# Performance work log

Measured on AMD Instinct MI355X. Metric: run time of the kernel, lower is better.

## Reference

```python
import jax, jax.numpy as jnp
import numpy as np

N_USERS = 200000
N_ITEMS = 100000
EMB_DIM = 64
N_LAYERS = 3
N_EDGES = 4000000
N_TOTAL = N_USERS + N_ITEMS


def setup_inputs() -> dict:
    key = jax.random.key(0)
    k1, k2, k3, k4 = jax.random.split(key, 4)
    # Xavier-uniform-ish init scale for embeddings
    lim = float(np.sqrt(6.0 / (N_USERS + EMB_DIM)))
    user_w = jax.random.uniform(k1, (N_USERS, EMB_DIM), jnp.float32, -lim, lim)
    lim_i = float(np.sqrt(6.0 / (N_ITEMS + EMB_DIM)))
    item_w = jax.random.uniform(k2, (N_ITEMS, EMB_DIM), jnp.float32, -lim_i, lim_i)
    src = jax.random.randint(k3, (N_EDGES,), 0, N_TOTAL, dtype=jnp.int32)
    dst = jax.random.randint(k4, (N_EDGES,), 0, N_TOTAL, dtype=jnp.int32)
    return {"user_w": user_w, "item_w": item_w, "src": src, "dst": dst}


def reference(user_w, item_w, src, dst):
    # x: [N_TOTAL, D] joint node embedding table
    x = jnp.concatenate([user_w, item_w], axis=0)
    # Row-degree of the COO adjacency (duplicates sum, same as coalesce)
    deg = jax.ops.segment_sum(jnp.ones_like(src, dtype=x.dtype), src,
                              num_segments=N_TOTAL)
    deg_inv_sqrt = jax.lax.rsqrt(deg + 1e-8)
    # Symmetric normalization weight per edge: d_i^-1/2 * d_j^-1/2
    w = (deg_inv_sqrt[src] * deg_inv_sqrt[dst])[:, None]  # [E, 1]

    h = x
    acc = x
    for _ in range(N_LAYERS):
        # SpMM: out[i] = sum_{(i,j) in E} w_ij * h[j]
        h = jax.ops.segment_sum(w * h[dst], src, num_segments=N_TOTAL)
        acc = acc + h
    out = acc / (N_LAYERS + 1)
    return out[:N_USERS], out[N_USERS:]
```

## Files before the change

kernel.cpp:

```cpp
#include <hip/hip_runtime.h>

#define N_USERS  200000
#define N_ITEMS  100000
#define N_TOTAL  300000
#define EMB_DIM  64
#define N_EDGES  4000000
#define N_LAYERS 3

#define SCAN_CHUNK 1024

#define B2_BITS 9
#define B2_ROWS (1 << B2_BITS)
#define NB2 ((N_TOTAL + B2_ROWS - 1) >> B2_BITS)
#define CHUNK_E 8192
#define NBLK ((N_EDGES + CHUNK_E - 1) / CHUNK_E)
#define NFLAT (NB2 * NBLK)
#define NSB_FLAT ((NFLAT + SCAN_CHUNK - 1) / SCAN_CHUNK)

#define DST_BITS 19
#define DST_MASK ((1 << DST_BITS) - 1)

typedef float f32x2 __attribute__((ext_vector_type(2)));

__device__ __forceinline__ unsigned bfpack(float a, float b) {
    unsigned ua = __float_as_uint(a); ua = (ua + 0x7fffu + ((ua >> 16) & 1u)) >> 16;
    unsigned ub = __float_as_uint(b); ub = (ub + 0x7fffu + ((ub >> 16) & 1u)) >> 16;
    return ua | (ub << 16);
}
__device__ __forceinline__ float bflo(unsigned u) { return __uint_as_float(u << 16); }
__device__ __forceinline__ float bfhi(unsigned u) { return __uint_as_float(u & 0xffff0000u); }
__device__ __forceinline__ f32x2 bf2(unsigned u) {
    f32x2 t; t.x = bflo(u); t.y = bfhi(u); return t;
}

__global__ void scanA_g(const int* __restrict__ in, int* __restrict__ out,
                        int* __restrict__ bsums, int n) {
    __shared__ int lds[256];
    int t = threadIdx.x, b = blockIdx.x;
    int base = b * SCAN_CHUNK + t * 4;
    int v[4];
#pragma unroll
    for (int k = 0; k < 4; ++k)
        v[k] = (base + k < n) ? in[base + k] : 0;
    int s = v[0] + v[1] + v[2] + v[3];
    lds[t] = s;
    __syncthreads();
    for (int off = 1; off < 256; off <<= 1) {
        int x = (t >= off) ? lds[t - off] : 0;
        __syncthreads();
        lds[t] += x;
        __syncthreads();
    }
    int inc = lds[t];
    int exc = inc - s;
    if (t == 255) bsums[b] = inc;
    int run = exc;
#pragma unroll
    for (int k = 0; k < 4; ++k) {
        if (base + k < n) out[base + k] = run;
        run += v[k];
    }
}

__global__ void scanB_g(int* __restrict__ bsums, int nb, int* __restrict__ total_out) {
    __shared__ int lds[512];
    int t = threadIdx.x;
    int v = (t < nb) ? bsums[t] : 0;
    lds[t] = v;
    __syncthreads();
    for (int o = 1; o < 512; o <<= 1) {
        int x = (t >= o) ? lds[t - o] : 0;
        __syncthreads();
        lds[t] += x;
        __syncthreads();
    }
    if (t < nb) bsums[t] = lds[t] - v;
    if (total_out && t == nb - 1) *total_out = lds[t];
}

__global__ void scanC_g(int* __restrict__ out, const int* __restrict__ bsums, int n) {
    int i = blockIdx.x * blockDim.x + threadIdx.x;
    if (i < n) out[i] += bsums[i >> 10];
}

__global__ __launch_bounds__(256) void partA_kernel(const int* __restrict__ src,
                                                    int* __restrict__ bcnt) {
    __shared__ int lcnt[NB2];
    int blk = blockIdx.x, t = threadIdx.x;
    for (int i = t; i < NB2; i += 256) lcnt[i] = 0;
    __syncthreads();
    int base = blk * CHUNK_E;
    int end = base + CHUNK_E; if (end > N_EDGES) end = N_EDGES;
    for (int e = base + t; e < end; e += 256)
        atomicAdd(&lcnt[src[e] >> B2_BITS], 1);
    __syncthreads();
    for (int i = t; i < NB2; i += 256)
        bcnt[(size_t)i * NBLK + blk] = lcnt[i];
}

__global__ __launch_bounds__(256) void partC_kernel(const int* __restrict__ src,
                                                    const int* __restrict__ dst,
                                                    const int* __restrict__ boffs,
                                                    int* __restrict__ edgebuf) {
    __shared__ int lcur[NB2];
    int blk = blockIdx.x, t = threadIdx.x;
    for (int i = t; i < NB2; i += 256) lcur[i] = boffs[(size_t)i * NBLK + blk];
    __syncthreads();
    int base = blk * CHUNK_E;
    int end = base + CHUNK_E; if (end > N_EDGES) end = N_EDGES;
    for (int e = base + t; e < end; e += 256) {
        int s = src[e], d = dst[e];
        int pos = atomicAdd(&lcur[s >> B2_BITS], 1);
        edgebuf[pos] = ((s & (B2_ROWS - 1)) << DST_BITS) | d;
    }
}

__global__ __launch_bounds__(256) void part2_kernel(const int* __restrict__ boffs,
                                                    const int* __restrict__ edgebuf,
                                                    int* __restrict__ col,
                                                    int* __restrict__ offs,
                                                    float* __restrict__ dinv) {
    __shared__ int lhist[B2_ROWS];
    __shared__ int lsums[256];
    int b = blockIdx.x;
    int base = b << B2_BITS;
    int nrows = N_TOTAL - base; if (nrows > B2_ROWS) nrows = B2_ROWS;
    int t = threadIdx.x;
    int bstart = boffs[(size_t)b * NBLK];
    int eend = (b + 1 < NB2) ? boffs[(size_t)(b + 1) * NBLK] : N_EDGES;

    for (int i = t; i < B2_ROWS; i += 256) lhist[i] = 0;
    __syncthreads();
    for (int j = bstart + t; j < eend; j += 256)
        atomicAdd(&lhist[edgebuf[j] >> DST_BITS], 1);
    __syncthreads();
    int v0 = lhist[2 * t], v1 = lhist[2 * t + 1];
    int s = v0 + v1;
    lsums[t] = s;
    __syncthreads();
    for (int o = 1; o < 256; o <<= 1) {
        int x = (t >= o) ? lsums[t - o] : 0;
        __syncthreads();
        lsums[t] += x;
        __syncthreads();
    }
    int exc = lsums[t] - s;
    int o0 = bstart + exc;
    int o1 = o0 + v0;
    if (2 * t < nrows) {
        offs[base + 2 * t] = o0;
        dinv[base + 2 * t] = rsqrtf((float)v0 + 1e-8f);
    }
    if (2 * t + 1 < nrows) {
        offs[base + 2 * t + 1] = o1;
        dinv[base + 2 * t + 1] = rsqrtf((float)v1 + 1e-8f);
    }
    if (b == NB2 - 1 && t == 0) offs[N_TOTAL] = N_EDGES;
    lhist[2 * t] = o0;
    lhist[2 * t + 1] = o1;
    __syncthreads();
    for (int j = bstart + t; j < eend; j += 256) {
        int e = edgebuf[j];
        int r = e >> DST_BITS;
        int pos = atomicAdd(&lhist[r], 1);
        col[pos] = e & DST_MASK;
    }
}

__global__ void convert_kernel(const float2* __restrict__ uw2,
                               const float2* __restrict__ iw2,
                               const float* __restrict__ dinv,
                               unsigned* __restrict__ g0) {
    int i = blockIdx.x * blockDim.x + threadIdx.x;
    const int n = (N_TOTAL + 1) * 32;
    if (i < n) {
        int row = i >> 5;
        if (row >= N_TOTAL) {
            g0[i] = 0u;
        } else {
            float2 x = (row < N_USERS) ? uw2[i] : iw2[i - N_USERS * 32];
            float di = dinv[row];
            g0[i] = bfpack(di * x.x, di * x.y);
        }
    }
}

template <int MODE>
__global__ __launch_bounds__(256) void gather_kernel(
        const int* __restrict__ offs,
        const int* __restrict__ col,
        const float* __restrict__ dinv,
        const unsigned* __restrict__ gprev,
        unsigned* __restrict__ gnext,
        float4* __restrict__ out4,
        const float4* __restrict__ uw4,
        const float4* __restrict__ iw4) {
    int row  = blockIdx.x * 4 + (threadIdx.x >> 6);
    int lane = threadIdx.x & 63;
    int q    = lane >> 4;
    int r    = lane & 15;
    int start = __builtin_amdgcn_readfirstlane(offs[row]);
    int end   = __builtin_amdgcn_readfirstlane(offs[row + 1]);
    f32x2 acc01 = {0.f, 0.f};
    f32x2 acc23 = {0.f, 0.f};
    for (int cb = start; cb < end; cb += 64) {
        int rem = end - cb;
        int n = rem > 64 ? 64 : rem;
        int myc = (lane < rem) ? col[cb + lane] : N_TOTAL;
        for (int k0 = 0; k0 < n; k0 += 8) {
            int c0 = __shfl(myc, k0 + q);
            int c1 = __shfl(myc, k0 + 4 + q);
            uint2 u0 = *(const uint2*)(gprev + ((size_t)(unsigned)c0 << 5) + 2 * r);
            uint2 u1 = *(const uint2*)(gprev + ((size_t)(unsigned)c1 << 5) + 2 * r);
            acc01 += bf2(u0.x); acc23 += bf2(u0.y);
            acc01 += bf2(u1.x); acc23 += bf2(u1.y);
        }
    }
    float a0 = acc01.x, a1 = acc01.y, a2 = acc23.x, a3 = acc23.y;
    a0 += __shfl_xor(a0, 16);
    a1 += __shfl_xor(a1, 16);
    a2 += __shfl_xor(a2, 16);
    a3 += __shfl_xor(a3, 16);
    a0 += __shfl_xor(a0, 32);
    a1 += __shfl_xor(a1, 32);
    a2 += __shfl_xor(a2, 32);
    a3 += __shfl_xor(a3, 32);
    if (lane < 16) {
        float di = dinv[row];
        float h0 = di * a0, h1 = di * a1, h2 = di * a2, h3 = di * a3;
        int p = row * 16 + r;
        if (MODE == 0) {
            float4 x = (row < N_USERS) ? uw4[p] : iw4[p - N_USERS * 16];
            ((uint2*)gnext)[p] = make_uint2(bfpack(di * h0, di * h1),
                                            bfpack(di * h2, di * h3));
            out4[p] = make_float4(x.x + h0, x.y + h1, x.z + h2, x.w + h3);
        } else if (MODE == 1) {
            float4 o = out4[p];
            ((uint2*)gnext)[p] = make_uint2(bfpack(di * h0, di * h1),
                                            bfpack(di * h2, di * h3));
            out4[p] = make_float4(o.x + h0, o.y + h1, o.z + h2, o.w + h3);
        } else {
            float4 o = out4[p];
            out4[p] = make_float4((o.x + h0) * 0.25f, (o.y + h1) * 0.25f,
                                  (o.z + h2) * 0.25f, (o.w + h3) * 0.25f);
        }
    }
    if (MODE != 2) {
        if (blockIdx.x == 0 && threadIdx.x < 32)
            gnext[N_TOTAL * 32 + threadIdx.x] = 0u;
    }
}

extern "C" void kernel_launch(void* const* d_in, const int* in_sizes, int n_in,
                              void* d_out, int out_size, void* d_ws, size_t ws_size,
                              hipStream_t stream) {
    const float* user_w = (const float*)d_in[0];
    const float* item_w = (const float*)d_in[1];
    const int*   src    = (const int*)d_in[2];
    const int*   dst    = (const int*)d_in[3];
    float* out = (float*)d_out;
    (void)in_sizes; (void)n_in; (void)out_size; (void)ws_size;

    char* ws = (char*)d_ws;
    size_t off = 0;
    auto alloc = [&](size_t bytes) {
        char* p = ws + off;
        off = (off + bytes + 255) & ~(size_t)255;
        return p;
    };
    int*      offs   = (int*)     alloc((size_t)(N_TOTAL + 1) * 4);
    int*      bcnt   = (int*)     alloc((size_t)NFLAT * 4);
    int*      boffs  = (int*)     alloc((size_t)NFLAT * 4);
    int*      bs2    = (int*)     alloc((size_t)NSB_FLAT * 4);
    int*      col    = (int*)     alloc((size_t)N_EDGES * 4);
    int*      edgebuf= (int*)     alloc((size_t)N_EDGES * 4);
    float*    dinv   = (float*)   alloc((size_t)N_TOTAL * 4);
    unsigned* g0     = (unsigned*)alloc((size_t)(N_TOTAL + 1) * 32 * 4);
    unsigned* g_a    = (unsigned*)alloc((size_t)(N_TOTAL + 1) * 32 * 4);
    unsigned* g_b    = (unsigned*)alloc((size_t)(N_TOTAL + 1) * 32 * 4);

    const int B = 256;
    const int gatherGrid = N_TOTAL / 4;

    partA_kernel<<<NBLK, B, 0, stream>>>(src, bcnt);
    scanA_g<<<NSB_FLAT, B, 0, stream>>>(bcnt, boffs, bs2, NFLAT);
    scanB_g<<<1, 512, 0, stream>>>(bs2, NSB_FLAT, nullptr);
    scanC_g<<<(NFLAT + B - 1) / B, B, 0, stream>>>(boffs, bs2, NFLAT);
    partC_kernel<<<NBLK, B, 0, stream>>>(src, dst, boffs, edgebuf);
    part2_kernel<<<NB2, B, 0, stream>>>(boffs, edgebuf, col, offs, dinv);

    convert_kernel<<<((N_TOTAL + 1) * 32 + B - 1) / B, B, 0, stream>>>(
        (const float2*)user_w, (const float2*)item_w, dinv, g0);

    const float4* uw4 = (const float4*)user_w;
    const float4* iw4 = (const float4*)item_w;
    float4* out4 = (float4*)out;
    gather_kernel<0><<<gatherGrid, B, 0, stream>>>(offs, col, dinv, g0,  g_a, out4, uw4, iw4);
    gather_kernel<1><<<gatherGrid, B, 0, stream>>>(offs, col, dinv, g_a, g_b, out4, uw4, iw4);
    gather_kernel<2><<<gatherGrid, B, 0, stream>>>(offs, col, dinv, g_b, nullptr, out4, uw4, iw4);
}
```

Baseline: 618.2 us.

## Vectorize partition loads, fold scan fixup into consumers, unroll gather wider

Removes the scanC kernel by adding the block-sum offset when partC and part2 read boffs. Moves partA, partC and part2 to 512-thread blocks with int4/int2 vectorized loads; part2 now handles one row per thread. Converts four floats per thread in convert_kernel, hoists the dinv load in gather, and unrolls the gather inner loop to four neighbour loads per step for more memory-level parallelism. The vector loads assume the edge arrays and chunk bases are suitably aligned and sized, and the wider unroll raises register pressure.

```diff
diff --git a/kernel.cpp b/kernel.cpp
--- a/kernel.cpp
+++ b/kernel.cpp
@@ -78,109 +78,114 @@
     if (total_out && t == nb - 1) *total_out = lds[t];
 }
 
-__global__ void scanC_g(int* __restrict__ out, const int* __restrict__ bsums, int n) {
-    int i = blockIdx.x * blockDim.x + threadIdx.x;
-    if (i < n) out[i] += bsums[i >> 10];
-}
-
-__global__ __launch_bounds__(256) void partA_kernel(const int* __restrict__ src,
+__global__ __launch_bounds__(512) void partA_kernel(const int* __restrict__ src,
                                                     int* __restrict__ bcnt) {
     __shared__ int lcnt[NB2];
     int blk = blockIdx.x, t = threadIdx.x;
-    for (int i = t; i < NB2; i += 256) lcnt[i] = 0;
+    for (int i = t; i < NB2; i += 512) lcnt[i] = 0;
     __syncthreads();
     int base = blk * CHUNK_E;
     int end = base + CHUNK_E; if (end > N_EDGES) end = N_EDGES;
-    for (int e = base + t; e < end; e += 256)
-        atomicAdd(&lcnt[src[e] >> B2_BITS], 1);
-    __syncthreads();
-    for (int i = t; i < NB2; i += 256)
+    for (int e = base + 4 * t; e < end; e += 4 * 512) {
+        int4 s4 = *(const int4*)(src + e);
+        atomicAdd(&lcnt[s4.x >> B2_BITS], 1);
+        atomicAdd(&lcnt[s4.y >> B2_BITS], 1);
+        atomicAdd(&lcnt[s4.z >> B2_BITS], 1);
+        atomicAdd(&lcnt[s4.w >> B2_BITS], 1);
+    }
+    __syncthreads();
+    for (int i = t; i < NB2; i += 512)
         bcnt[(size_t)i * NBLK + blk] = lcnt[i];
 }
 
-__global__ __launch_bounds__(256) void partC_kernel(const int* __restrict__ src,
+__global__ __launch_bounds__(512) void partC_kernel(const int* __restrict__ src,
                                                     const int* __restrict__ dst,
                                                     const int* __restrict__ boffs,
+                                                    const int* __restrict__ bs2,
                                                     int* __restrict__ edgebuf) {
     __shared__ int lcur[NB2];
     int blk = blockIdx.x, t = threadIdx.x;
-    for (int i = t; i < NB2; i += 256) lcur[i] = boffs[(size_t)i * NBLK + blk];
+    for (int i = t; i < NB2; i += 512) {
+        size_t f = (size_t)i * NBLK + blk;
+        lcur[i] = boffs[f] + bs2[f >> 10];
+    }
     __syncthreads();
     int base = blk * CHUNK_E;
     int end = base + CHUNK_E; if (end > N_EDGES) end = N_EDGES;
-    for (int e = base + t; e < end; e += 256) {
-        int s = src[e], d = dst[e];
-        int pos = atomicAdd(&lcur[s >> B2_BITS], 1);
-        edgebuf[pos] = ((s & (B2_ROWS - 1)) << DST_BITS) | d;
-    }
-}
-
-__global__ __launch_bounds__(256) void part2_kernel(const int* __restrict__ boffs,
+    for (int e = base + 2 * t; e < end; e += 2 * 512) {
+        int2 s2 = *(const int2*)(src + e);
+        int2 d2 = *(const int2*)(dst + e);
+        int pos0 = atomicAdd(&lcur[s2.x >> B2_BITS], 1);
+        edgebuf[pos0] = ((s2.x & (B2_ROWS - 1)) << DST_BITS) | d2.x;
+        int pos1 = atomicAdd(&lcur[s2.y >> B2_BITS], 1);
+        edgebuf[pos1] = ((s2.y & (B2_ROWS - 1)) << DST_BITS) | d2.y;
+    }
+}
+
+__global__ __launch_bounds__(512) void part2_kernel(const int* __restrict__ boffs,
+                                                    const int* __restrict__ bs2,
                                                     const int* __restrict__ edgebuf,
                                                     int* __restrict__ col,
                                                     int* __restrict__ offs,
                                                     float* __restrict__ dinv) {
     __shared__ int lhist[B2_ROWS];
-    __shared__ int lsums[256];
+    __shared__ int lsums[512];
     int b = blockIdx.x;
     int base = b << B2_BITS;
     int nrows = N_TOTAL - base; if (nrows > B2_ROWS) nrows = B2_ROWS;
     int t = threadIdx.x;
-    int bstart = boffs[(size_t)b * NBLK];
-    int eend = (b + 1 < NB2) ? boffs[(size_t)(b + 1) * NBLK] : N_EDGES;
-
-    for (int i = t; i < B2_ROWS; i += 256) lhist[i] = 0;
-    __syncthreads();
-    for (int j = bstart + t; j < eend; j += 256)
+    size_t f0 = (size_t)b * NBLK;
+    int bstart = boffs[f0] + bs2[f0 >> 10];
+    int eend;
+    if (b + 1 < NB2) {
+        size_t f1 = (size_t)(b + 1) * NBLK;
+        eend = boffs[f1] + bs2[f1 >> 10];
+    } else eend = N_EDGES;
+
+    if (t < B2_ROWS) lhist[t] = 0;
+    __syncthreads();
+    for (int j = bstart + t; j < eend; j += 512)
         atomicAdd(&lhist[edgebuf[j] >> DST_BITS], 1);
     __syncthreads();
-    int v0 = lhist[2 * t], v1 = lhist[2 * t + 1];
-    int s = v0 + v1;
-    lsums[t] = s;
-    __syncthreads();
-    for (int o = 1; o < 256; o <<= 1) {
+    int v = lhist[t];
+    lsums[t] = v;
+    __syncthreads();
+    for (int o = 1; o < 512; o <<= 1) {
         int x = (t >= o) ? lsums[t - o] : 0;
         __syncthreads();
         lsums[t] += x;
         __syncthreads();
     }
-    int exc = lsums[t] - s;
-    int o0 = bstart + exc;
-    int o1 = o0 + v0;
-    if (2 * t < nrows) {
-        offs[base + 2 * t] = o0;
-        dinv[base + 2 * t] = rsqrtf((float)v0 + 1e-8f);
-    }
-    if (2 * t + 1 < nrows) {
-        offs[base + 2 * t + 1] = o1;
-        dinv[base + 2 * t + 1] = rsqrtf((float)v1 + 1e-8f);
+    int o0 = bstart + lsums[t] - v;
+    if (t < nrows) {
+        offs[base + t] = o0;
+        dinv[base + t] = rsqrtf((float)v + 1e-8f);
     }
     if (b == NB2 - 1 && t == 0) offs[N_TOTAL] = N_EDGES;
-    lhist[2 * t] = o0;
-    lhist[2 * t + 1] = o1;
-    __syncthreads();
-    for (int j = bstart + t; j < eend; j += 256) {
+    lhist[t] = o0;
+    __syncthreads();
+    for (int j = bstart + t; j < eend; j += 512) {
         int e = edgebuf[j];
-        int r = e >> DST_BITS;
-        int pos = atomicAdd(&lhist[r], 1);
+        int pos = atomicAdd(&lhist[e >> DST_BITS], 1);
         col[pos] = e & DST_MASK;
     }
 }
 
-__global__ void convert_kernel(const float2* __restrict__ uw2,
-                               const float2* __restrict__ iw2,
+__global__ void convert_kernel(const float4* __restrict__ uw4,
+                               const float4* __restrict__ iw4,
                                const float* __restrict__ dinv,
-                               unsigned* __restrict__ g0) {
+                               uint2* __restrict__ g0) {
     int i = blockIdx.x * blockDim.x + threadIdx.x;
-    const int n = (N_TOTAL + 1) * 32;
+    const int n = (N_TOTAL + 1) * 16;
     if (i < n) {
-        int row = i >> 5;
+        int row = i >> 4;
         if (row >= N_TOTAL) {
-            g0[i] = 0u;
+            g0[i] = make_uint2(0u, 0u);
         } else {
-            float2 x = (row < N_USERS) ? uw2[i] : iw2[i - N_USERS * 32];
+            float4 x = (row < N_USERS) ? uw4[i] : iw4[i - N_USERS * 16];
             float di = dinv[row];
-            g0[i] = bfpack(di * x.x, di * x.y);
+            g0[i] = make_uint2(bfpack(di * x.x, di * x.y),
+                               bfpack(di * x.z, di * x.w));
         }
     }
 }
@@ -201,19 +206,26 @@
     int r    = lane & 15;
     int start = __builtin_amdgcn_readfirstlane(offs[row]);
     int end   = __builtin_amdgcn_readfirstlane(offs[row + 1]);
+    float di  = dinv[row];
     f32x2 acc01 = {0.f, 0.f};
     f32x2 acc23 = {0.f, 0.f};
     for (int cb = start; cb < end; cb += 64) {
         int rem = end - cb;
         int n = rem > 64 ? 64 : rem;
         int myc = (lane < rem) ? col[cb + lane] : N_TOTAL;
-        for (int k0 = 0; k0 < n; k0 += 8) {
+        for (int k0 = 0; k0 < n; k0 += 16) {
             int c0 = __shfl(myc, k0 + q);
             int c1 = __shfl(myc, k0 + 4 + q);
+            int c2 = __shfl(myc, k0 + 8 + q);
+            int c3 = __shfl(myc, k0 + 12 + q);
             uint2 u0 = *(const uint2*)(gprev + ((size_t)(unsigned)c0 << 5) + 2 * r);
             uint2 u1 = *(const uint2*)(gprev + ((size_t)(unsigned)c1 << 5) + 2 * r);
+            uint2 u2 = *(const uint2*)(gprev + ((size_t)(unsigned)c2 << 5) + 2 * r);
+            uint2 u3 = *(const uint2*)(gprev + ((size_t)(unsigned)c3 << 5) + 2 * r);
             acc01 += bf2(u0.x); acc23 += bf2(u0.y);
             acc01 += bf2(u1.x); acc23 += bf2(u1.y);
+            acc01 += bf2(u2.x); acc23 += bf2(u2.y);
+            acc01 += bf2(u3.x); acc23 += bf2(u3.y);
         }
     }
     float a0 = acc01.x, a1 = acc01.y, a2 = acc23.x, a3 = acc23.y;
@@ -226,7 +238,6 @@
     a2 += __shfl_xor(a2, 32);
     a3 += __shfl_xor(a3, 32);
     if (lane < 16) {
-        float di = dinv[row];
         float h0 = di * a0, h1 = di * a1, h2 = di * a2, h3 = di * a3;
         int p = row * 16 + r;
         if (MODE == 0) {
@@ -282,15 +293,14 @@
     const int B = 256;
     const int gatherGrid = N_TOTAL / 4;
 
-    partA_kernel<<<NBLK, B, 0, stream>>>(src, bcnt);
+    partA_kernel<<<NBLK, 512, 0, stream>>>(src, bcnt);
     scanA_g<<<NSB_FLAT, B, 0, stream>>>(bcnt, boffs, bs2, NFLAT);
     scanB_g<<<1, 512, 0, stream>>>(bs2, NSB_FLAT, nullptr);
-    scanC_g<<<(NFLAT + B - 1) / B, B, 0, stream>>>(boffs, bs2, NFLAT);
-    partC_kernel<<<NBLK, B, 0, stream>>>(src, dst, boffs, edgebuf);
-    part2_kernel<<<NB2, B, 0, stream>>>(boffs, edgebuf, col, offs, dinv);
-
-    convert_kernel<<<((N_TOTAL + 1) * 32 + B - 1) / B, B, 0, stream>>>(
-        (const float2*)user_w, (const float2*)item_w, dinv, g0);
+    partC_kernel<<<NBLK, 512, 0, stream>>>(src, dst, boffs, bs2, edgebuf);
+    part2_kernel<<<NB2, 512, 0, stream>>>(boffs, bs2, edgebuf, col, offs, dinv);
+
+    convert_kernel<<<((N_TOTAL + 1) * 16 + B - 1) / B, B, 0, stream>>>(
+        (const float4*)user_w, (const float4*)item_w, dinv, (uint2*)g0);
 
     const float4* uw4 = (const float4*)user_w;
     const float4* iw4 = (const float4*)item_w;
```

After: 573.9 us. 1.08x faster.
